# Optimization experiments

Measured on AMD Instinct MI355X. Metric: run time of the kernel, lower is better.

The kernel has to match this reference:

```python
import jax, jax.numpy as jnp
import numpy as np
from functools import partial

DELTA_B = 30.0
DELTA_H = 30.0
NB = 12  # 360/30
NH = 12
E, H, A, MLP, T = 16, 32, 32, 128, 20


def setup_inputs() -> dict:
    key = jax.random.key(0)
    ks = jax.random.split(key, 32)
    B, N = 512, 32
    inp = {}
    inp['x'] = jax.random.normal(ks[0], (B, N, T, 2), jnp.float32)
    inp['dmat'] = jax.random.uniform(ks[1], (B, N, T, N), jnp.float32) * 10.0
    inp['bmat'] = jax.random.uniform(ks[2], (B, N, T, N), jnp.float32) * 360.0
    inp['hmat'] = jax.random.uniform(ks[3], (B, N, T, N), jnp.float32) * 360.0
    inp['mask'] = jnp.ones((B, N, T), jnp.float32)
    g = lambda k, sh, s=0.1: jax.random.normal(k, sh, jnp.float32) * s
    inp['emb_w'] = g(ks[4], (2, E)); inp['emb_b'] = jnp.zeros((E,), jnp.float32)
    inp['w_ih'] = g(ks[5], (E, 4 * H)); inp['w_hh'] = g(ks[6], (H, 4 * H))
    inp['b_ih'] = jnp.zeros((4 * H,), jnp.float32); inp['b_hh'] = jnp.zeros((4 * H,), jnp.float32)
    inp['enc2att_w'] = g(ks[7], (H, A)); inp['enc2att_b'] = jnp.zeros((A,), jnp.float32)
    inp['domain_tab'] = jnp.full((NB, NH), 5.0, jnp.float32)  # domain_parameter init
    inp['spemb_w'] = g(ks[8], (2 * A, A)); inp['spemb_b'] = jnp.zeros((A,), jnp.float32)
    inp['att2enc_w'] = g(ks[9], (A, H)); inp['att2enc_b'] = jnp.zeros((H,), jnp.float32)
    inp['cls_w1'] = g(ks[10], (T * H, MLP)); inp['cls_b1'] = jnp.zeros((MLP,), jnp.float32)
    inp['cls_w2'] = g(ks[11], (MLP, MLP)); inp['cls_b2'] = jnp.zeros((MLP,), jnp.float32)
    inp['cls_w3'] = g(ks[12], (MLP, 1)); inp['cls_b3'] = jnp.zeros((1,), jnp.float32)
    return inp


def _forward(x, dmat, bmat, hmat, mask, emb_w, emb_b, w_ih, w_hh, b_ih, b_hh,
             enc2att_w, enc2att_b, domain_tab, spemb_w, spemb_b,
             att2enc_w, att2enc_b, cls_w1, cls_b1, cls_w2, cls_b2, cls_w3, cls_b3):
    B, N = x.shape[0], x.shape[1]
    xe = x @ emb_w + emb_b                      # [B,N,T,E]
    # time-major sequences for scan
    seq = (jnp.moveaxis(xe, 2, 0), jnp.moveaxis(dmat, 2, 0), jnp.moveaxis(bmat, 2, 0),
           jnp.moveaxis(hmat, 2, 0), jnp.moveaxis(mask, 2, 0))
    h0 = jnp.zeros((B, N, H), xe.dtype)
    c0 = jnp.zeros((B, N, H), xe.dtype)

    def step(carry, inp):
        h, c = carry
        x_t, d_t, b_t, hd_t, m_t = inp
        gates = x_t @ w_ih + h @ w_hh + (b_ih + b_hh)   # [B,N,4H]
        i, f, g, o = jnp.split(gates, 4, axis=-1)
        c_new = jax.nn.sigmoid(f) * c + jax.nn.sigmoid(i) * jnp.tanh(g)
        h_lstm = jax.nn.sigmoid(o) * jnp.tanh(c_new)
        ha = h_lstm @ enc2att_w + enc2att_b              # enc2att -> [B,N,A]
        # spatial attention: domain value from bearing/heading bins vs distance
        ib = jnp.clip(jnp.floor(b_t / DELTA_B), 0, NB - 1).astype(jnp.int32)
        ih = jnp.clip(jnp.floor(hd_t / DELTA_H), 0, NH - 1).astype(jnp.int32)
        w = jax.nn.relu(domain_tab[ib, ih] - d_t)        # [B,N,N]
        w = w * m_t[:, :, None] * m_t[:, None, :]
        w = w / (w.sum(-1, keepdims=True) + 1e-8)
        att = jnp.einsum('bij,bjd->bid', w, ha)          # neighbor-weighted hidden
        emb = jnp.tanh(jnp.concatenate([ha, att], -1) @ spemb_w + spemb_b)
        h_new = emb @ att2enc_w + att2enc_b              # back to hidden_size
        return (h_new, c_new), h_new

    (_, _), hs = jax.lax.scan(step, (h0, c0), seq)       # hs: [T,B,N,H]
    enc = jnp.moveaxis(hs, 0, 2).reshape(B, N, T * H)
    z = jax.nn.leaky_relu(enc @ cls_w1 + cls_b1, 0.2)
    z = jax.nn.leaky_relu(z @ cls_w2 + cls_b2, 0.2)
    return jax.nn.sigmoid(z @ cls_w3 + cls_b3)           # [B,N,1]


def reference(x, dmat, bmat, hmat, mask, emb_w, emb_b, w_ih, w_hh, b_ih, b_hh,
              enc2att_w, enc2att_b, domain_tab, spemb_w, spemb_b,
              att2enc_w, att2enc_b, cls_w1, cls_b1, cls_w2, cls_b2, cls_w3, cls_b3):
    return _forward(x, dmat, bmat, hmat, mask, emb_w, emb_b, w_ih, w_hh, b_ih, b_hh,
                    enc2att_w, enc2att_b, domain_tab, spemb_w, spemb_b,
                    att2enc_w, att2enc_b, cls_w1, cls_b1, cls_w2, cls_b2, cls_w3, cls_b3)
```

## Files before the change

### kernel.cpp

```cpp
#include <hip/hip_runtime.h>
#include <hip/hip_bf16.h>

#define TD_B 512
#define TD_N 32
#define TD_T 20

typedef __bf16 bf16x8 __attribute__((ext_vector_type(8)));
typedef __bf16 bf16x4 __attribute__((ext_vector_type(4)));
typedef float  f32x4  __attribute__((ext_vector_type(4)));

#define MFMA(a, b, c) __builtin_amdgcn_mfma_f32_16x16x32_bf16((a), (b), (c), 0, 0, 0)

__device__ __forceinline__ float sigf(float x)  { return 1.0f / (1.0f + __expf(-x)); }
__device__ __forceinline__ float tanhf_(float x){ return 2.0f / (1.0f + __expf(-2.0f * x)) - 1.0f; }

extern "C" __global__ void __launch_bounds__(256, 2)
traj_disc_kernel(const float* __restrict__ x, const float* __restrict__ dmat,
                 const float* __restrict__ bmat, const float* __restrict__ hmat,
                 const float* __restrict__ mask,
                 const float* __restrict__ emb_w, const float* __restrict__ emb_b,
                 const float* __restrict__ w_ih, const float* __restrict__ w_hh,
                 const float* __restrict__ b_ih, const float* __restrict__ b_hh,
                 const float* __restrict__ e2a_w, const float* __restrict__ e2a_b,
                 const float* __restrict__ dom,
                 const float* __restrict__ sp_w, const float* __restrict__ sp_b,
                 const float* __restrict__ a2e_w, const float* __restrict__ a2e_b,
                 const float* __restrict__ w1, const float* __restrict__ b1,
                 const float* __restrict__ w2, const float* __restrict__ b2,
                 const float* __restrict__ w3, const float* __restrict__ b3,
                 float* __restrict__ out)
{
    const int b   = blockIdx.x;
    const int tid = threadIdx.x;
    const int lane = tid & 63;
    const int w    = tid >> 6;
    const int l15  = lane & 15;
    const int lg   = lane >> 4;

    __shared__ __bf16 sAin[32][80];
    __shared__ float  sGate[32][136];
    __shared__ __bf16 sHl[32][40];
    __shared__ __bf16 sPA[32][80];
    __shared__ __bf16 sHaT[32][40];
    __shared__ __bf16 sEmb[32][40];
    __shared__ float  sWmat[32][36];
    __shared__ __bf16 sWN[32][40];
    __shared__ float  sMask[32][21];
    __shared__ float  sMcur[32];
    __shared__ float  sDom[144];
    __shared__ float  sEmbW[3][16];
    __shared__ float  sBias4[128];
    __shared__ float  sBiasE[32], sBiasS[32], sBiasA[32];

    for (int idx = tid; idx < 32 * 80; idx += 256) (&sAin[0][0])[idx] = (__bf16)0.0f;
    for (int idx = tid; idx < 640; idx += 256) {
        int n = idx / 20, tt = idx % 20;
        sMask[n][tt] = mask[(b * TD_N + n) * TD_T + tt];
    }
    if (tid < 144) sDom[tid] = dom[tid];
    if (tid < 32)  sEmbW[tid >> 4][tid & 15] = emb_w[tid];
    if (tid >= 32 && tid < 48) sEmbW[2][tid - 32] = emb_b[tid - 32];
    if (tid < 128) { int hh = tid >> 2, g = tid & 3; sBias4[tid] = b_ih[g * 32 + hh] + b_hh[g * 32 + hh]; }
    if (tid < 32) { sBiasE[tid] = e2a_b[tid]; sBiasS[tid] = sp_b[tid]; sBiasA[tid] = a2e_b[tid]; }

    bf16x8 Bg[2][2];
    #pragma unroll
    for (int kt = 0; kt < 2; ++kt)
        #pragma unroll
        for (int ntp = 0; ntp < 2; ++ntp) {
            int c = (2 * w + ntp) * 16 + l15;
            int cg = (c & 3) * 32 + (c >> 2);
            #pragma unroll
            for (int j = 0; j < 8; ++j) {
                int row = kt * 32 + lg * 8 + j;
                float v = (row < 16) ? w_ih[row * 128 + cg]
                         : (row < 48) ? w_hh[(row - 16) * 128 + cg] : 0.0f;
                Bg[kt][ntp][j] = (__bf16)v;
            }
        }
    const int mtw = w >> 1, ntw = w & 1;
    const int cw  = ntw * 16 + l15;
    bf16x8 Be2a, Ba2e, Bsp[2];
    #pragma unroll
    for (int j = 0; j < 8; ++j) {
        int row = lg * 8 + j;
        Be2a[j] = (__bf16)e2a_w[row * 32 + cw];
        Ba2e[j] = (__bf16)a2e_w[row * 32 + cw];
    }
    #pragma unroll
    for (int kt = 0; kt < 2; ++kt)
        #pragma unroll
        for (int j = 0; j < 8; ++j)
            Bsp[kt][j] = (__bf16)sp_w[(kt * 32 + lg * 8 + j) * 32 + cw];

    const int hI = tid & 31, nb = tid >> 5;
    float cst[4] = {0.f, 0.f, 0.f, 0.f};
    f32x4 accZ[2][2] = {};

    __syncthreads();

    for (int t = 0; t < TD_T; ++t) {
        bf16x8 Bw1[2];
        if (t >= 1) {
            #pragma unroll
            for (int ntp = 0; ntp < 2; ++ntp) {
                int c = (2 * w + ntp) * 16 + l15;
                #pragma unroll
                for (int j = 0; j < 8; ++j)
                    Bw1[ntp][j] = (__bf16)w1[((t - 1) * 32 + lg * 8 + j) * 128 + c];
            }
        }
        {
            int i = tid >> 3, p = tid & 7;
            int base = ((b * TD_N + i) * TD_T + t) * TD_N + 4 * p;
            float4 dv = *(const float4*)(dmat + base);
            float4 bv = *(const float4*)(bmat + base);
            float4 hv = *(const float4*)(hmat + base);
            float4 wv;
            #pragma unroll
            for (int q = 0; q < 4; ++q) {
                float bq = (&bv.x)[q], hq = (&hv.x)[q];
                int ib = (int)floorf(bq * (1.0f / 30.0f)); ib = ib < 0 ? 0 : (ib > 11 ? 11 : ib);
                int ih = (int)floorf(hq * (1.0f / 30.0f)); ih = ih < 0 ? 0 : (ih > 11 ? 11 : ih);
                float v = sDom[ib * 12 + ih] - (&dv.x)[q];
                (&wv.x)[q] = v > 0.f ? v : 0.f;
            }
            *(float4*)&sWmat[i][4 * p] = wv;
        }
        {
            int n = tid >> 3, e2 = tid & 7;
            float x0 = x[((b * TD_N + n) * TD_T + t) * 2 + 0];
            float x1 = x[((b * TD_N + n) * TD_T + t) * 2 + 1];
            #pragma unroll
            for (int q = 0; q < 2; ++q) {
                int e = 2 * e2 + q;
                sAin[n][e] = (__bf16)(x0 * sEmbW[0][e] + x1 * sEmbW[1][e] + sEmbW[2][e]);
            }
        }
        if (tid < 32) sMcur[tid] = sMask[tid][t];
        __syncthreads();

        #pragma unroll
        for (int mt = 0; mt < 2; ++mt) {
            bf16x8 a0 = *(const bf16x8*)&sAin[mt * 16 + l15][lg * 8];
            bf16x8 a1 = *(const bf16x8*)&sAin[mt * 16 + l15][32 + lg * 8];
            #pragma unroll
            for (int ntp = 0; ntp < 2; ++ntp) {
                f32x4 cc = {0.f, 0.f, 0.f, 0.f};
                cc = MFMA(a0, Bg[0][ntp], cc);
                cc = MFMA(a1, Bg[1][ntp], cc);
                int c = (2 * w + ntp) * 16 + l15;
                #pragma unroll
                for (int q = 0; q < 4; ++q)
                    sGate[mt * 16 + lg * 4 + q][c] = cc[q];
            }
        }
        if (t >= 1) {
            #pragma unroll
            for (int mt = 0; mt < 2; ++mt) {
                bf16x8 ah = *(const bf16x8*)&sAin[mt * 16 + l15][16 + lg * 8];
                #pragma unroll
                for (int ntp = 0; ntp < 2; ++ntp)
                    accZ[mt][ntp] = MFMA(ah, Bw1[ntp], accZ[mt][ntp]);
            }
        }
        {
            int i = tid >> 3, p = tid & 7;
            float4 wv = *(const float4*)&sWmat[i][4 * p];
            float4 mj = *(const float4*)&sMcur[4 * p];
            float  mi = sMcur[i];
            float s = wv.x * mj.x + wv.y * mj.y + wv.z * mj.z + wv.w * mj.w;
            s += __shfl_xor(s, 1); s += __shfl_xor(s, 2); s += __shfl_xor(s, 4);
            float inv = mi / (mi * s + 1e-8f);
            #pragma unroll
            for (int q = 0; q < 4; ++q)
                sWN[i][4 * p + q] = (__bf16)((&wv.x)[q] * (&mj.x)[q] * inv);
        }
        __syncthreads();

        {
            float4 bb = *(const float4*)&sBias4[4 * hI];
            #pragma unroll
            for (int r = 0; r < 4; ++r) {
                int n = nb + 8 * r;
                float4 gv = *(const float4*)&sGate[n][4 * hI];
                float gi = gv.x + bb.x, gf = gv.y + bb.y, gg = gv.z + bb.z, go = gv.w + bb.w;
                float cn = sigf(gf) * cst[r] + sigf(gi) * tanhf_(gg);
                cst[r] = cn;
                sHl[n][hI] = (__bf16)(sigf(go) * tanhf_(cn));
            }
        }
        __syncthreads();

        {
            bf16x8 a = *(const bf16x8*)&sHl[mtw * 16 + l15][lg * 8];
            f32x4 cc = {0.f, 0.f, 0.f, 0.f};
            cc = MFMA(a, Be2a, cc);
            float bias = sBiasE[cw];
            bf16x4 tv;
            #pragma unroll
            for (int q = 0; q < 4; ++q) {
                float v = cc[q] + bias;
                sPA[mtw * 16 + lg * 4 + q][cw] = (__bf16)v;
                tv[q] = (__bf16)v;
            }
            *(bf16x4*)&sHaT[cw][mtw * 16 + lg * 4] = tv;
        }
        __syncthreads();

        {
            bf16x8 a  = *(const bf16x8*)&sWN[mtw * 16 + l15][lg * 8];
            bf16x8 bb = *(const bf16x8*)&sHaT[cw][lg * 8];
            f32x4 cc = {0.f, 0.f, 0.f, 0.f};
            cc = MFMA(a, bb, cc);
            #pragma unroll
            for (int q = 0; q < 4; ++q)
                sPA[mtw * 16 + lg * 4 + q][32 + cw] = (__bf16)cc[q];
        }
        __syncthreads();

        {
            bf16x8 a0 = *(const bf16x8*)&sPA[mtw * 16 + l15][lg * 8];
            bf16x8 a1 = *(const bf16x8*)&sPA[mtw * 16 + l15][32 + lg * 8];
            f32x4 cc = {0.f, 0.f, 0.f, 0.f};
            cc = MFMA(a0, Bsp[0], cc);
            cc = MFMA(a1, Bsp[1], cc);
            float bias = sBiasS[cw];
            #pragma unroll
            for (int q = 0; q < 4; ++q)
                sEmb[mtw * 16 + lg * 4 + q][cw] = (__bf16)tanhf_(cc[q] + bias);
        }
        __syncthreads();

        {
            bf16x8 a = *(const bf16x8*)&sEmb[mtw * 16 + l15][lg * 8];
            f32x4 cc = {0.f, 0.f, 0.f, 0.f};
            cc = MFMA(a, Ba2e, cc);
            float bias = sBiasA[cw];
            #pragma unroll
            for (int q = 0; q < 4; ++q)
                sAin[mtw * 16 + lg * 4 + q][16 + cw] = (__bf16)(cc[q] + bias);
        }
        __syncthreads();
    }

    {
        bf16x8 Bw1[2];
        #pragma unroll
        for (int ntp = 0; ntp < 2; ++ntp) {
            int c = (2 * w + ntp) * 16 + l15;
            #pragma unroll
            for (int j = 0; j < 8; ++j)
                Bw1[ntp][j] = (__bf16)w1[(19 * 32 + lg * 8 + j) * 128 + c];
        }
        #pragma unroll
        for (int mt = 0; mt < 2; ++mt) {
            bf16x8 ah = *(const bf16x8*)&sAin[mt * 16 + l15][16 + lg * 8];
            #pragma unroll
            for (int ntp = 0; ntp < 2; ++ntp)
                accZ[mt][ntp] = MFMA(ah, Bw1[ntp], accZ[mt][ntp]);
        }
    }
    __bf16* z1bf = (__bf16*)&sGate[0][0];
    __bf16* z2bf = z1bf + 32 * 136;
    #pragma unroll
    for (int mt = 0; mt < 2; ++mt)
        #pragma unroll
        for (int ntp = 0; ntp < 2; ++ntp) {
            int c = (2 * w + ntp) * 16 + l15;
            float bias = b1[c];
            #pragma unroll
            for (int q = 0; q < 4; ++q) {
                float v = accZ[mt][ntp][q] + bias;
                v = v > 0.f ? v : 0.2f * v;
                z1bf[(mt * 16 + lg * 4 + q) * 136 + c] = (__bf16)v;
            }
        }
    __syncthreads();

    {
        f32x4 c2[2][2] = {};
        #pragma unroll
        for (int kt = 0; kt < 4; ++kt) {
            bf16x8 a[2];
            #pragma unroll
            for (int mt = 0; mt < 2; ++mt)
                a[mt] = *(const bf16x8*)&z1bf[(mt * 16 + l15) * 136 + kt * 32 + lg * 8];
            bf16x8 bb[2];
            #pragma unroll
            for (int ntp = 0; ntp < 2; ++ntp) {
                int c = (2 * w + ntp) * 16 + l15;
                #pragma unroll
                for (int j = 0; j < 8; ++j)
                    bb[ntp][j] = (__bf16)w2[(kt * 32 + lg * 8 + j) * 128 + c];
            }
            #pragma unroll
            for (int mt = 0; mt < 2; ++mt)
                #pragma unroll
                for (int ntp = 0; ntp < 2; ++ntp)
                    c2[mt][ntp] = MFMA(a[mt], bb[ntp], c2[mt][ntp]);
        }
        #pragma unroll
        for (int mt = 0; mt < 2; ++mt)
            #pragma unroll
            for (int ntp = 0; ntp < 2; ++ntp) {
                int c = (2 * w + ntp) * 16 + l15;
                float bias = b2[c];
                #pragma unroll
                for (int q = 0; q < 4; ++q) {
                    float v = c2[mt][ntp][q] + bias;
                    v = v > 0.f ? v : 0.2f * v;
                    z2bf[(mt * 16 + lg * 4 + q) * 136 + c] = (__bf16)v;
                }
            }
    }
    __syncthreads();

    {
        int n = tid >> 3, kg = tid & 7;
        bf16x8 v0 = *(const bf16x8*)&z2bf[n * 136 + kg * 16];
        bf16x8 v1 = *(const bf16x8*)&z2bf[n * 136 + kg * 16 + 8];
        float s = 0.f;
        #pragma unroll
        for (int j = 0; j < 8; ++j)
            s += (float)v0[j] * w3[kg * 16 + j] + (float)v1[j] * w3[kg * 16 + 8 + j];
        s += __shfl_xor(s, 1); s += __shfl_xor(s, 2); s += __shfl_xor(s, 4);
        if (kg == 0) out[b * TD_N + n] = 1.0f / (1.0f + __expf(-(s + b3[0])));
    }
}

extern "C" void kernel_launch(void* const* d_in, const int* in_sizes, int n_in,
                              void* d_out, int out_size, void* d_ws, size_t ws_size,
                              hipStream_t stream) {
    (void)in_sizes; (void)n_in; (void)d_ws; (void)ws_size; (void)out_size;
    const float* x     = (const float*)d_in[0];
    const float* dmat  = (const float*)d_in[1];
    const float* bmat  = (const float*)d_in[2];
    const float* hmat  = (const float*)d_in[3];
    const float* mask  = (const float*)d_in[4];
    const float* emb_w = (const float*)d_in[5];
    const float* emb_b = (const float*)d_in[6];
    const float* w_ih  = (const float*)d_in[7];
    const float* w_hh  = (const float*)d_in[8];
    const float* b_ih  = (const float*)d_in[9];
    const float* b_hh  = (const float*)d_in[10];
    const float* e2a_w = (const float*)d_in[11];
    const float* e2a_b = (const float*)d_in[12];
    const float* dom   = (const float*)d_in[13];
    const float* sp_w  = (const float*)d_in[14];
    const float* sp_b  = (const float*)d_in[15];
    const float* a2e_w = (const float*)d_in[16];
    const float* a2e_b = (const float*)d_in[17];
    const float* w1    = (const float*)d_in[18];
    const float* b1    = (const float*)d_in[19];
    const float* w2    = (const float*)d_in[20];
    const float* b2    = (const float*)d_in[21];
    const float* w3    = (const float*)d_in[22];
    const float* b3    = (const float*)d_in[23];
    float* out = (float*)d_out;

    traj_disc_kernel<<<dim3(TD_B), dim3(256), 0, stream>>>(
        x, dmat, bmat, hmat, mask, emb_w, emb_b, w_ih, w_hh, b_ih, b_hh,
        e2a_w, e2a_b, dom, sp_w, sp_b, a2e_w, a2e_b,
        w1, b1, w2, b2, w3, b3, out);
}
```

Before: 80.13 us.

## Replicate small per-step GEMM chain per wave to eliminate block barriers

Each wave now redundantly computes the full 32x32 attention/embedding chain (e2a, neighbor attention, spatial embedding, a2e) in private shared-memory buffers. This removes four of the six per-timestep block-wide barriers. The change also prefetches next-step dmat/bmat/hmat/x into registers, folds the weight-normalisation into the pre-barrier phase, and moves biases and embedding weights from shared memory into registers. The cost is four times the MFMA work on those small GEMMs, plus extra LDS and register pressure that could limit occupancy.

```diff
diff --git a/kernel.cpp b/kernel.cpp
--- a/kernel.cpp
+++ b/kernel.cpp
@@ -2,8 +2,6 @@
 #include <hip/hip_bf16.h>
 
 #define TD_B 512
-#define TD_N 32
-#define TD_T 20
 
 typedef __bf16 bf16x8 __attribute__((ext_vector_type(8)));
 typedef __bf16 bf16x4 __attribute__((ext_vector_type(4)));
@@ -38,30 +36,40 @@
     const int lg   = lane >> 4;
 
     __shared__ __bf16 sAin[32][80];
-    __shared__ float  sGate[32][136];
+    __shared__ __align__(16) char sGateBuf[17408];
     __shared__ __bf16 sHl[32][40];
-    __shared__ __bf16 sPA[32][80];
-    __shared__ __bf16 sHaT[32][40];
-    __shared__ __bf16 sEmb[32][40];
-    __shared__ float  sWmat[32][36];
     __shared__ __bf16 sWN[32][40];
-    __shared__ float  sMask[32][21];
-    __shared__ float  sMcur[32];
+    __shared__ float  sMaskT[20][36];
     __shared__ float  sDom[144];
-    __shared__ float  sEmbW[3][16];
-    __shared__ float  sBias4[128];
-    __shared__ float  sBiasE[32], sBiasS[32], sBiasA[32];
+    __shared__ __bf16 sPAv [4][32][72];
+    __shared__ __bf16 sHaTv[4][32][40];
+    __shared__ __bf16 sEmbv[4][32][40];
+
+    float (*sGate)[132] = (float (*)[132])sGateBuf;
+    __bf16 (*sPA)[72]  = sPAv[w];
+    __bf16 (*sHaT)[40] = sHaTv[w];
+    __bf16 (*sEmb)[40] = sEmbv[w];
 
     for (int idx = tid; idx < 32 * 80; idx += 256) (&sAin[0][0])[idx] = (__bf16)0.0f;
     for (int idx = tid; idx < 640; idx += 256) {
-        int n = idx / 20, tt = idx % 20;
-        sMask[n][tt] = mask[(b * TD_N + n) * TD_T + tt];
+        int tt = idx >> 5, n = idx & 31;
+        sMaskT[tt][n] = mask[(b * 32 + n) * 20 + tt];
     }
     if (tid < 144) sDom[tid] = dom[tid];
-    if (tid < 32)  sEmbW[tid >> 4][tid & 15] = emb_w[tid];
-    if (tid >= 32 && tid < 48) sEmbW[2][tid - 32] = emb_b[tid - 32];
-    if (tid < 128) { int hh = tid >> 2, g = tid & 3; sBias4[tid] = b_ih[g * 32 + hh] + b_hh[g * 32 + hh]; }
-    if (tid < 32) { sBiasE[tid] = e2a_b[tid]; sBiasS[tid] = sp_b[tid]; sBiasA[tid] = a2e_b[tid]; }
+
+    const int i0 = tid >> 3, p0 = tid & 7;
+    const int hI = tid & 31, nb = tid >> 5;
+    const float ewa0 = emb_w[2 * p0],      ewa1 = emb_w[2 * p0 + 1];
+    const float ewb0 = emb_w[16 + 2 * p0], ewb1 = emb_w[16 + 2 * p0 + 1];
+    const float eb0  = emb_b[2 * p0],      eb1  = emb_b[2 * p0 + 1];
+    float4 bb4;
+    bb4.x = b_ih[hI] + b_hh[hI];
+    bb4.y = b_ih[32 + hI] + b_hh[32 + hI];
+    bb4.z = b_ih[64 + hI] + b_hh[64 + hI];
+    bb4.w = b_ih[96 + hI] + b_hh[96 + hI];
+    const float bE[2] = { e2a_b[l15], e2a_b[16 + l15] };
+    const float bS[2] = { sp_b[l15],  sp_b[16 + l15] };
+    const float bA[2] = { a2e_b[l15], a2e_b[16 + l15] };
 
     bf16x8 Bg[2][2];
     #pragma unroll
@@ -78,68 +86,73 @@
                 Bg[kt][ntp][j] = (__bf16)v;
             }
         }
-    const int mtw = w >> 1, ntw = w & 1;
-    const int cw  = ntw * 16 + l15;
-    bf16x8 Be2a, Ba2e, Bsp[2];
+    bf16x8 Be2aF[2], Ba2eF[2], BspF[2][2];
     #pragma unroll
-    for (int j = 0; j < 8; ++j) {
-        int row = lg * 8 + j;
-        Be2a[j] = (__bf16)e2a_w[row * 32 + cw];
-        Ba2e[j] = (__bf16)a2e_w[row * 32 + cw];
-    }
-    #pragma unroll
-    for (int kt = 0; kt < 2; ++kt)
-        #pragma unroll
-        for (int j = 0; j < 8; ++j)
-            Bsp[kt][j] = (__bf16)sp_w[(kt * 32 + lg * 8 + j) * 32 + cw];
-
-    const int hI = tid & 31, nb = tid >> 5;
+    for (int nt2 = 0; nt2 < 2; ++nt2) {
+        int c2 = nt2 * 16 + l15;
+        #pragma unroll
+        for (int j = 0; j < 8; ++j) {
+            int row = lg * 8 + j;
+            Be2aF[nt2][j] = (__bf16)e2a_w[row * 32 + c2];
+            Ba2eF[nt2][j] = (__bf16)a2e_w[row * 32 + c2];
+        }
+        #pragma unroll
+        for (int kt = 0; kt < 2; ++kt)
+            #pragma unroll
+            for (int j = 0; j < 8; ++j)
+                BspF[kt][nt2][j] = (__bf16)sp_w[(kt * 32 + lg * 8 + j) * 32 + c2];
+    }
+
     float cst[4] = {0.f, 0.f, 0.f, 0.f};
     f32x4 accZ[2][2] = {};
-
+    bf16x8 Bw1cur[2];
+
+    float4 pdv, pbv, phv; float px0, px1;
+    {
+        int base = ((b * 32 + i0) * 20 + 0) * 32 + 4 * p0;
+        pdv = *(const float4*)(dmat + base);
+        pbv = *(const float4*)(bmat + base);
+        phv = *(const float4*)(hmat + base);
+        int xb = ((b * 32 + i0) * 20 + 0) * 2;
+        px0 = x[xb]; px1 = x[xb + 1];
+    }
     __syncthreads();
 
-    for (int t = 0; t < TD_T; ++t) {
-        bf16x8 Bw1[2];
-        if (t >= 1) {
-            #pragma unroll
-            for (int ntp = 0; ntp < 2; ++ntp) {
-                int c = (2 * w + ntp) * 16 + l15;
-                #pragma unroll
-                for (int j = 0; j < 8; ++j)
-                    Bw1[ntp][j] = (__bf16)w1[((t - 1) * 32 + lg * 8 + j) * 128 + c];
-            }
-        }
-        {
-            int i = tid >> 3, p = tid & 7;
-            int base = ((b * TD_N + i) * TD_T + t) * TD_N + 4 * p;
-            float4 dv = *(const float4*)(dmat + base);
-            float4 bv = *(const float4*)(bmat + base);
-            float4 hv = *(const float4*)(hmat + base);
-            float4 wv;
-            #pragma unroll
-            for (int q = 0; q < 4; ++q) {
-                float bq = (&bv.x)[q], hq = (&hv.x)[q];
-                int ib = (int)floorf(bq * (1.0f / 30.0f)); ib = ib < 0 ? 0 : (ib > 11 ? 11 : ib);
-                int ih = (int)floorf(hq * (1.0f / 30.0f)); ih = ih < 0 ? 0 : (ih > 11 ? 11 : ih);
-                float v = sDom[ib * 12 + ih] - (&dv.x)[q];
-                (&wv.x)[q] = v > 0.f ? v : 0.f;
-            }
-            *(float4*)&sWmat[i][4 * p] = wv;
-        }
-        {
-            int n = tid >> 3, e2 = tid & 7;
-            float x0 = x[((b * TD_N + n) * TD_T + t) * 2 + 0];
-            float x1 = x[((b * TD_N + n) * TD_T + t) * 2 + 1];
-            #pragma unroll
-            for (int q = 0; q < 2; ++q) {
-                int e = 2 * e2 + q;
-                sAin[n][e] = (__bf16)(x0 * sEmbW[0][e] + x1 * sEmbW[1][e] + sEmbW[2][e]);
-            }
-        }
-        if (tid < 32) sMcur[tid] = sMask[tid][t];
+    #pragma unroll 1
+    for (int t = 0; t < 20; ++t) {
+        float4 dv = pdv, bv = pbv, hv = phv;
+        float xx0 = px0, xx1 = px1;
+        if (t < 19) {
+            int base = ((b * 32 + i0) * 20 + (t + 1)) * 32 + 4 * p0;
+            pdv = *(const float4*)(dmat + base);
+            pbv = *(const float4*)(bmat + base);
+            phv = *(const float4*)(hmat + base);
+            int xb = ((b * 32 + i0) * 20 + (t + 1)) * 2;
+            px0 = x[xb]; px1 = x[xb + 1];
+        }
+        float4 mj = *(const float4*)&sMaskT[t][4 * p0];
+        float  mi = sMaskT[t][i0];
+        float wq[4];
+        #pragma unroll
+        for (int q = 0; q < 4; ++q) {
+            float bq = (&bv.x)[q], hq = (&hv.x)[q];
+            int ib = (int)floorf(bq * (1.0f / 30.0f)); ib = ib < 0 ? 0 : (ib > 11 ? 11 : ib);
+            int ih = (int)floorf(hq * (1.0f / 30.0f)); ih = ih < 0 ? 0 : (ih > 11 ? 11 : ih);
+            float v = sDom[ib * 12 + ih] - (&dv.x)[q];
+            v = v > 0.f ? v : 0.f;
+            wq[q] = v * (&mj.x)[q];
+        }
+        float s = wq[0] + wq[1] + wq[2] + wq[3];
+        s += __shfl_xor(s, 1); s += __shfl_xor(s, 2); s += __shfl_xor(s, 4);
+        float inv = mi / (mi * s + 1e-8f);
+        bf16x4 wn4;
+        #pragma unroll
+        for (int q = 0; q < 4; ++q) wn4[q] = (__bf16)(wq[q] * inv);
+        sAin[i0][2 * p0]     = (__bf16)(xx0 * ewa0 + xx1 * ewb0 + eb0);
+        sAin[i0][2 * p0 + 1] = (__bf16)(xx0 * ewa1 + xx1 * ewb1 + eb1);
         __syncthreads();
 
+        *(bf16x4*)&sWN[i0][4 * p0] = wn4;
         #pragma unroll
         for (int mt = 0; mt < 2; ++mt) {
             bf16x8 a0 = *(const bf16x8*)&sAin[mt * 16 + l15][lg * 8];
@@ -161,107 +174,101 @@
                 bf16x8 ah = *(const bf16x8*)&sAin[mt * 16 + l15][16 + lg * 8];
                 #pragma unroll
                 for (int ntp = 0; ntp < 2; ++ntp)
-                    accZ[mt][ntp] = MFMA(ah, Bw1[ntp], accZ[mt][ntp]);
-            }
-        }
-        {
-            int i = tid >> 3, p = tid & 7;
-            float4 wv = *(const float4*)&sWmat[i][4 * p];
-            float4 mj = *(const float4*)&sMcur[4 * p];
-            float  mi = sMcur[i];
-            float s = wv.x * mj.x + wv.y * mj.y + wv.z * mj.z + wv.w * mj.w;
-            s += __shfl_xor(s, 1); s += __shfl_xor(s, 2); s += __shfl_xor(s, 4);
-            float inv = mi / (mi * s + 1e-8f);
-            #pragma unroll
-            for (int q = 0; q < 4; ++q)
-                sWN[i][4 * p + q] = (__bf16)((&wv.x)[q] * (&mj.x)[q] * inv);
-        }
-        __syncthreads();
-
-        {
-            float4 bb = *(const float4*)&sBias4[4 * hI];
-            #pragma unroll
-            for (int r = 0; r < 4; ++r) {
-                int n = nb + 8 * r;
-                float4 gv = *(const float4*)&sGate[n][4 * hI];
-                float gi = gv.x + bb.x, gf = gv.y + bb.y, gg = gv.z + bb.z, go = gv.w + bb.w;
-                float cn = sigf(gf) * cst[r] + sigf(gi) * tanhf_(gg);
-                cst[r] = cn;
-                sHl[n][hI] = (__bf16)(sigf(go) * tanhf_(cn));
-            }
-        }
-        __syncthreads();
-
-        {
-            bf16x8 a = *(const bf16x8*)&sHl[mtw * 16 + l15][lg * 8];
-            f32x4 cc = {0.f, 0.f, 0.f, 0.f};
-            cc = MFMA(a, Be2a, cc);
-            float bias = sBiasE[cw];
-            bf16x4 tv;
-            #pragma unroll
-            for (int q = 0; q < 4; ++q) {
-                float v = cc[q] + bias;
-                sPA[mtw * 16 + lg * 4 + q][cw] = (__bf16)v;
-                tv[q] = (__bf16)v;
-            }
-            *(bf16x4*)&sHaT[cw][mtw * 16 + lg * 4] = tv;
-        }
-        __syncthreads();
-
-        {
-            bf16x8 a  = *(const bf16x8*)&sWN[mtw * 16 + l15][lg * 8];
-            bf16x8 bb = *(const bf16x8*)&sHaT[cw][lg * 8];
-            f32x4 cc = {0.f, 0.f, 0.f, 0.f};
-            cc = MFMA(a, bb, cc);
-            #pragma unroll
-            for (int q = 0; q < 4; ++q)
-                sPA[mtw * 16 + lg * 4 + q][32 + cw] = (__bf16)cc[q];
-        }
-        __syncthreads();
-
-        {
-            bf16x8 a0 = *(const bf16x8*)&sPA[mtw * 16 + l15][lg * 8];
-            bf16x8 a1 = *(const bf16x8*)&sPA[mtw * 16 + l15][32 + lg * 8];
-            f32x4 cc = {0.f, 0.f, 0.f, 0.f};
-            cc = MFMA(a0, Bsp[0], cc);
-            cc = MFMA(a1, Bsp[1], cc);
-            float bias = sBiasS[cw];
-            #pragma unroll
-            for (int q = 0; q < 4; ++q)
-                sEmb[mtw * 16 + lg * 4 + q][cw] = (__bf16)tanhf_(cc[q] + bias);
-        }
-        __syncthreads();
-
-        {
-            bf16x8 a = *(const bf16x8*)&sEmb[mtw * 16 + l15][lg * 8];
-            f32x4 cc = {0.f, 0.f, 0.f, 0.f};
-            cc = MFMA(a, Ba2e, cc);
-            float bias = sBiasA[cw];
-            #pragma unroll
-            for (int q = 0; q < 4; ++q)
-                sAin[mtw * 16 + lg * 4 + q][16 + cw] = (__bf16)(cc[q] + bias);
-        }
-        __syncthreads();
-    }
-
-    {
-        bf16x8 Bw1[2];
+                    accZ[mt][ntp] = MFMA(ah, Bw1cur[ntp], accZ[mt][ntp]);
+            }
+        }
         #pragma unroll
         for (int ntp = 0; ntp < 2; ++ntp) {
             int c = (2 * w + ntp) * 16 + l15;
             #pragma unroll
             for (int j = 0; j < 8; ++j)
-                Bw1[ntp][j] = (__bf16)w1[(19 * 32 + lg * 8 + j) * 128 + c];
-        }
-        #pragma unroll
-        for (int mt = 0; mt < 2; ++mt) {
-            bf16x8 ah = *(const bf16x8*)&sAin[mt * 16 + l15][16 + lg * 8];
-            #pragma unroll
-            for (int ntp = 0; ntp < 2; ++ntp)
-                accZ[mt][ntp] = MFMA(ah, Bw1[ntp], accZ[mt][ntp]);
-        }
-    }
-    __bf16* z1bf = (__bf16*)&sGate[0][0];
+                Bw1cur[ntp][j] = (__bf16)w1[(t * 32 + lg * 8 + j) * 128 + c];
+        }
+        __syncthreads();
+
+        #pragma unroll
+        for (int r = 0; r < 4; ++r) {
+            int n = nb + 8 * r;
+            float4 gv = *(const float4*)&sGate[n][4 * hI];
+            float gi = gv.x + bb4.x, gf = gv.y + bb4.y, gg = gv.z + bb4.z, go = gv.w + bb4.w;
+            float cn = sigf(gf) * cst[r] + sigf(gi) * tanhf_(gg);
+            cst[r] = cn;
+            sHl[n][hI] = (__bf16)(sigf(go) * tanhf_(cn));
+        }
+        __syncthreads();
+
+        f32x4 haC[2][2];
+        #pragma unroll
+        for (int mt2 = 0; mt2 < 2; ++mt2) {
+            bf16x8 a = *(const bf16x8*)&sHl[mt2 * 16 + l15][lg * 8];
+            #pragma unroll
+            for (int nt2 = 0; nt2 < 2; ++nt2) {
+                f32x4 cc = {0.f, 0.f, 0.f, 0.f};
+                haC[mt2][nt2] = MFMA(a, Be2aF[nt2], cc);
+            }
+        }
+        #pragma unroll
+        for (int mt2 = 0; mt2 < 2; ++mt2)
+            #pragma unroll
+            for (int nt2 = 0; nt2 < 2; ++nt2) {
+                bf16x4 tv;
+                #pragma unroll
+                for (int q = 0; q < 4; ++q) {
+                    float v = haC[mt2][nt2][q] + bE[nt2];
+                    sPA[mt2 * 16 + lg * 4 + q][nt2 * 16 + l15] = (__bf16)v;
+                    tv[q] = (__bf16)v;
+                }
+                *(bf16x4*)&sHaT[nt2 * 16 + l15][mt2 * 16 + lg * 4] = tv;
+            }
+        #pragma unroll
+        for (int mt2 = 0; mt2 < 2; ++mt2) {
+            bf16x8 aW = *(const bf16x8*)&sWN[mt2 * 16 + l15][lg * 8];
+            #pragma unroll
+            for (int nt2 = 0; nt2 < 2; ++nt2) {
+                bf16x8 bT = *(const bf16x8*)&sHaT[nt2 * 16 + l15][lg * 8];
+                f32x4 cc = {0.f, 0.f, 0.f, 0.f};
+                cc = MFMA(aW, bT, cc);
+                #pragma unroll
+                for (int q = 0; q < 4; ++q)
+                    sPA[mt2 * 16 + lg * 4 + q][32 + nt2 * 16 + l15] = (__bf16)cc[q];
+            }
+        }
+        #pragma unroll
+        for (int mt2 = 0; mt2 < 2; ++mt2) {
+            bf16x8 a0 = *(const bf16x8*)&sPA[mt2 * 16 + l15][lg * 8];
+            bf16x8 a1 = *(const bf16x8*)&sPA[mt2 * 16 + l15][32 + lg * 8];
+            #pragma unroll
+            for (int nt2 = 0; nt2 < 2; ++nt2) {
+                f32x4 cc = {0.f, 0.f, 0.f, 0.f};
+                cc = MFMA(a0, BspF[0][nt2], cc);
+                cc = MFMA(a1, BspF[1][nt2], cc);
+                #pragma unroll
+                for (int q = 0; q < 4; ++q)
+                    sEmb[mt2 * 16 + lg * 4 + q][nt2 * 16 + l15] = (__bf16)tanhf_(cc[q] + bS[nt2]);
+            }
+        }
+        #pragma unroll
+        for (int mt2 = 0; mt2 < 2; ++mt2) {
+            bf16x8 a = *(const bf16x8*)&sEmb[mt2 * 16 + l15][lg * 8];
+            #pragma unroll
+            for (int nt2 = 0; nt2 < 2; ++nt2) {
+                f32x4 cc = {0.f, 0.f, 0.f, 0.f};
+                cc = MFMA(a, Ba2eF[nt2], cc);
+                #pragma unroll
+                for (int q = 0; q < 4; ++q)
+                    sAin[mt2 * 16 + lg * 4 + q][16 + nt2 * 16 + l15] = (__bf16)(cc[q] + bA[nt2]);
+            }
+        }
+    }
+
+    #pragma unroll
+    for (int mt = 0; mt < 2; ++mt) {
+        bf16x8 ah = *(const bf16x8*)&sAin[mt * 16 + l15][16 + lg * 8];
+        #pragma unroll
+        for (int ntp = 0; ntp < 2; ++ntp)
+            accZ[mt][ntp] = MFMA(ah, Bw1cur[ntp], accZ[mt][ntp]);
+    }
+    __bf16* z1bf = (__bf16*)sGateBuf;
     __bf16* z2bf = z1bf + 32 * 136;
     #pragma unroll
     for (int mt = 0; mt < 2; ++mt)
@@ -325,7 +332,7 @@
         for (int j = 0; j < 8; ++j)
             s += (float)v0[j] * w3[kg * 16 + j] + (float)v1[j] * w3[kg * 16 + 8 + j];
         s += __shfl_xor(s, 1); s += __shfl_xor(s, 2); s += __shfl_xor(s, 4);
-        if (kg == 0) out[b * TD_N + n] = 1.0f / (1.0f + __expf(-(s + b3[0])));
+        if (kg == 0) out[b * 32 + n] = 1.0f / (1.0f + __expf(-(s + b3[0])));
     }
 }
 
```

Result: slower. 103.0 us (+28.6%).
